# Optimization experiments

Hardware: AMD Instinct MI355X
Metric: run time of the kernel (lower is better)

## Reference

```python
import jax, jax.numpy as jnp
import numpy as np


def _cdist(a, b):
    # a: [B, N, D], b: [B, M, D] -> [B, N, M] Euclidean distances
    sq = (jnp.sum(a * a, -1)[:, :, None]
          + jnp.sum(b * b, -1)[:, None, :]
          - 2.0 * jnp.einsum('bnd,bmd->bnm', a, b))
    return jnp.sqrt(jnp.maximum(sq, 1e-12))


def setup_inputs() -> dict:
    key = jax.random.key(0)
    k1, k2, k3, k4 = jax.random.split(key, 4)
    B, N, NC, S = 2, 32768, 1024, 32
    centers = jax.random.normal(k1, (B, NC, 3), dtype=jnp.float32)
    radius = jax.random.uniform(k2, (B, NC, 1), dtype=jnp.float32)
    xyz = jax.random.normal(k3, (B, N, 3), dtype=jnp.float32)
    sphere_points = jax.random.normal(k4, (B, NC * S, 3), dtype=jnp.float32)
    return {"centers": centers, "radius": radius, "xyz": xyz,
            "sphere_points": sphere_points}


def reference(centers, radius, xyz, sphere_points):
    B, NC, _ = centers.shape
    # point -> center distances  [B, N, NC]
    dmat = _cdist(xyz, centers)
    cd_p_to_c = jnp.min(dmat, axis=-1)            # [B, N]
    idx_p_to_c = jnp.argmin(dmat, axis=-1)        # [B, N]
    # gather radius of nearest center for each point
    radius_from_p = jnp.take_along_axis(radius[..., 0], idx_p_to_c, axis=1)  # [B, N]
    # is_surface=False branch: clamp positive diffs to 0, then mean(|.|)
    diff = jnp.minimum(radius_from_p - cd_p_to_c, 0.0)
    radius_difference_p_to_c = jnp.mean(jnp.abs(diff), axis=1)               # [B]
    # sphere-point -> sample distances  [B, N, NC*S]
    dmat_sp = _cdist(xyz, sphere_points)
    cd_sp_to_p = jnp.min(dmat_sp, axis=1)          # [B, NC*S]
    max_cd_sp_to_p = jnp.max(cd_sp_to_p.reshape(B, NC, -1), axis=-1)         # [B, NC]
    radius_difference_c_to_p = jnp.mean(jnp.abs(max_cd_sp_to_p), axis=1)     # [B]
    res = radius_difference_c_to_p + radius_difference_p_to_c
    return jnp.mean(res)  # reduction='mean'
```

## Files before the change

### kernel.cpp

```cpp
#include <hip/hip_runtime.h>

#define B   2
#define N   32768
#define NC  1024
#define S   32
#define NSP (NC * S)

#define CHUNK 1024
#define NCH   (N / CHUNK)
#define BLKT  512
#define FR    4
#define COLS_BLK (8 * FR * 32)
#define GRIDX (NSP / COLS_BLK)

#define PJ  2
#define CSL 128

typedef __attribute__((ext_vector_type(8)))  short short8v;
typedef __attribute__((ext_vector_type(16))) float f32x16;
typedef const __attribute__((address_space(1))) void gvoid_t;
typedef __attribute__((address_space(3))) void svoid_t;

static __device__ __forceinline__ unsigned short f2b(float x) {
    unsigned u = __float_as_uint(x);
    return (unsigned short)((u + 0x7FFFu + ((u >> 16) & 1u)) >> 16);
}
static __device__ __forceinline__ float b2f(unsigned short u) {
    return __uint_as_float(((unsigned)u) << 16);
}
static __device__ __forceinline__ float min3f(float a, float b, float c) {
    return fminf(fminf(a, b), c);
}


__global__ __launch_bounds__(256) void k_prep(const float* __restrict__ xyz,
                                              unsigned short* __restrict__ Afrag,
                                              unsigned long long* __restrict__ best,
                                              unsigned* __restrict__ minsq,
                                              unsigned* __restrict__ accw) {
    int i = blockIdx.x * 256 + threadIdx.x;
    if (i < 2) accw[i] = 0u;
    best[i]  = ~0ull;
    minsq[i] = 0x7F800000u;

    const float* q = xyz + (size_t)i * 3;
    float qx = q[0], qy = q[1], qz = q[2];
    float h = 0.5f * (qx * qx + qy * qy + qz * qz);
    unsigned short xh = f2b(-qx), yh = f2b(-qy), zh = f2b(-qz);
    unsigned short xl = f2b(-qx - b2f(xh));
    unsigned short yl = f2b(-qy - b2f(yh));
    unsigned short zl = f2b(-qz - b2f(zh));
    unsigned short hh = f2b(h), hl = f2b(h - b2f(hh));

    int b = i >> 15, j = i & (N - 1);
    int tile = j >> 5, r = j & 31;
    unsigned short* base = Afrag + ((size_t)b * N + (size_t)tile * 32) * 16;
    uint4 s0, s1;
    s0.x = (unsigned)xh | ((unsigned)yh << 16);
    s0.y = (unsigned)zh | ((unsigned)xl << 16);
    s0.z = (unsigned)yl | ((unsigned)zl << 16);
    s0.w = (unsigned)xh | ((unsigned)yh << 16);
    s1.x = (unsigned)zh | ((unsigned)hh << 16);
    s1.y = (unsigned)hl;
    s1.z = 0u; s1.w = 0u;
    *(uint4*)(base + (size_t)r * 8)        = s0;
    *(uint4*)(base + (size_t)(r + 32) * 8) = s1;
}

__global__ __launch_bounds__(256) void k_p2c(const float* __restrict__ centers,
                                             const float* __restrict__ xyz,
                                             unsigned long long* __restrict__ best) {
    __shared__ float4 c4[CSL];
    const int b = blockIdx.z, qb = blockIdx.y, tid = threadIdx.x;

    const float* cb = centers + ((size_t)b * NC + qb * CSL) * 3;
    for (int g = tid; g < CSL / 4; g += 256) {
        float4 f0 = ((const float4*)cb)[g * 3 + 0];
        float4 f1 = ((const float4*)cb)[g * 3 + 1];
        float4 f2 = ((const float4*)cb)[g * 3 + 2];
        float x0 = f0.x, y0 = f0.y, z0 = f0.z;
        float x1 = f0.w, y1 = f1.x, z1 = f1.y;
        float x2 = f1.z, y2 = f1.w, z2 = f2.x;
        float x3 = f2.y, y3 = f2.z, z3 = f2.w;
        c4[g * 4 + 0] = make_float4(x0, y0, z0, 0.5f * (x0 * x0 + y0 * y0 + z0 * z0));
        c4[g * 4 + 1] = make_float4(x1, y1, z1, 0.5f * (x1 * x1 + y1 * y1 + z1 * z1));
        c4[g * 4 + 2] = make_float4(x2, y2, z2, 0.5f * (x2 * x2 + y2 * y2 + z2 * z2));
        c4[g * 4 + 3] = make_float4(x3, y3, z3, 0.5f * (x3 * x3 + y3 * y3 + z3 * z3));
    }
    __syncthreads();

    const int pbase = blockIdx.x * (256 * PJ) + tid;
    float px[PJ], py[PJ], pz[PJ], tmin[PJ];
    int imin[PJ];
    #pragma unroll
    for (int k = 0; k < PJ; ++k) {
        const float* p = xyz + ((size_t)b * N + pbase + k * 256) * 3;
        px[k] = p[0]; py[k] = p[1]; pz[k] = p[2];
        tmin[k] = 1e30f; imin[k] = 0;
    }

    #pragma unroll 4
    for (int c = 0; c < CSL; ++c) {
        float4 q = c4[c];
        #pragma unroll
        for (int k = 0; k < PJ; ++k) {
            float t = q.w - px[k] * q.x - py[k] * q.y - pz[k] * q.z;
            bool lt = t < tmin[k];
            tmin[k] = lt ? t : tmin[k];
            imin[k] = lt ? c : imin[k];
        }
    }

    #pragma unroll
    for (int k = 0; k < PJ; ++k) {
        unsigned bits = __float_as_uint(tmin[k]);
        unsigned ord  = (bits & 0x80000000u) ? ~bits : (bits | 0x80000000u);
        unsigned long long key =
            ((unsigned long long)ord << 32) | (unsigned)(qb * CSL + imin[k]);
        atomicMin(best + (size_t)b * N + pbase + k * 256, key);
    }
}

__global__ __launch_bounds__(BLKT) void k_sp2p(const float* __restrict__ sp,
                                               const unsigned short* __restrict__ Afrag,
                                               unsigned* __restrict__ minsq) {
    __shared__ unsigned short lds[CHUNK * 16];
    const int b = blockIdx.z, chunk = blockIdx.y;
    const int tid = threadIdx.x, wid = tid >> 6, lane = tid & 63;

    const char* src = (const char*)(Afrag +
                        ((size_t)b * N + (size_t)chunk * CHUNK) * 16);
    #pragma unroll
    for (int it = 0; it < 4; ++it) {
        int off = it * 8192 + wid * 1024;
        __builtin_amdgcn_global_load_lds((gvoid_t*)(src + off + lane * 16),
                                         (svoid_t*)((char*)lds + off), 16, 0, 0);
    }

    const int colbase = blockIdx.x * COLS_BLK + wid * (FR * 32) + (lane & 31);
    float pp[FR]; short8v bf[FR];
    #pragma unroll
    for (int f = 0; f < FR; ++f) {
        const float* p = sp + ((size_t)b * NSP + colbase + f * 32) * 3;
        float qx = p[0], qy = p[1], qz = p[2];
        pp[f] = qx * qx + qy * qy + qz * qz;
        unsigned short xh = f2b(qx), yh = f2b(qy), zh = f2b(qz);
        unsigned short xl = f2b(qx - b2f(xh));
        unsigned short yl = f2b(qy - b2f(yh));
        unsigned short zl = f2b(qz - b2f(zh));
        short8v v;
        if (lane < 32) {
            v[0] = (short)xh; v[1] = (short)yh; v[2] = (short)zh;
            v[3] = (short)xh; v[4] = (short)yh; v[5] = (short)zh;
            v[6] = (short)xl; v[7] = (short)yl;
        } else {
            v[0] = (short)zl; v[1] = (short)0x3F80; v[2] = (short)0x3F80;
            v[3] = 0; v[4] = 0; v[5] = 0; v[6] = 0; v[7] = 0;
        }
        bf[f] = v;
    }
    f32x16 zero;
    #pragma unroll
    for (int i = 0; i < 16; ++i) zero[i] = 0.0f;

    float run[FR];
    #pragma unroll
    for (int f = 0; f < FR; ++f) run[f] = 1e30f;

    __syncthreads();

    const unsigned short* ap = lds + lane * 8;
    #pragma unroll 2
    for (int t = 0; t < CHUNK / 32; ++t) {
        short8v a = *(const short8v*)(ap + (size_t)t * 512);
        #pragma unroll
        for (int f = 0; f < FR; ++f) {
            f32x16 d = __builtin_amdgcn_mfma_f32_32x32x16_bf16(a, bf[f], zero, 0, 0, 0);
            float r0 = min3f(d[0],  d[1],  d[2]);
            float r1 = min3f(d[3],  d[4],  d[5]);
            float r2 = min3f(d[6],  d[7],  d[8]);
            float r3 = min3f(d[9],  d[10], d[11]);
            float r4 = min3f(d[12], d[13], d[14]);
            float r5 = min3f(r0, r1, d[15]);
            float r6 = min3f(r2, r3, r4);
            run[f] = min3f(run[f], r5, r6);
        }
    }

    #pragma unroll
    for (int f = 0; f < FR; ++f)
        run[f] = fminf(run[f], __shfl_xor(run[f], 32, 64));
    if (lane < 32) {
        unsigned* mb = minsq + (size_t)b * NSP + colbase;
        #pragma unroll
        for (int f = 0; f < FR; ++f) {
            float sq = fmaxf(2.0f * run[f] + pp[f], 0.0f);
            atomicMin(mb + f * 32, __float_as_uint(sq));
        }
    }
}

__global__ __launch_bounds__(256) void k_fin(const unsigned long long* __restrict__ best,
                                             const unsigned* __restrict__ minsq,
                                             const float* __restrict__ xyz,
                                             const float* __restrict__ radius,
                                             float* __restrict__ acc,
                                             unsigned* __restrict__ counter,
                                             float* __restrict__ out) {
    const int tid = threadIdx.x;
    const int i = blockIdx.x * 256 + tid;
    const int b = i >> 15;

    unsigned long long k = best[i];
    int idx = (int)(k & 0xFFFFFFFFu);
    unsigned ord  = (unsigned)(k >> 32);
    unsigned bits = (ord & 0x80000000u) ? (ord ^ 0x80000000u) : ~ord;
    float tmin = __uint_as_float(bits);
    const float* p = xyz + (size_t)i * 3;
    float pp = p[0] * p[0] + p[1] * p[1] + p[2] * p[2];
    float cdp = sqrtf(fmaxf(2.0f * tmin + pp, 1e-12f));
    float val = fmaxf(cdp - radius[(size_t)b * NC + idx], 0.0f);

    float cd = sqrtf(fmaxf(__uint_as_float(minsq[i]), 1e-12f));
    #pragma unroll
    for (int o = 16; o > 0; o >>= 1) cd = fmaxf(cd, __shfl_xor(cd, o, 64));

    float contrib = val * (1.0f / N) +
                    (((tid & 31) == 0) ? cd * (1.0f / NC) : 0.0f);
    #pragma unroll
    for (int o = 32; o > 0; o >>= 1) contrib += __shfl_down(contrib, o);
    __shared__ float wsum[4];
    if ((tid & 63) == 0) wsum[tid >> 6] = contrib;
    __syncthreads();
    if (tid == 0) atomicAdd(&acc[0], wsum[0] + wsum[1] + wsum[2] + wsum[3]);

    __shared__ int lastf;
    if (tid == 0) {
        __threadfence();
        unsigned old = atomicAdd(counter, 1u);
        lastf = (old == (unsigned)(gridDim.x - 1));
    }
    __syncthreads();
    if (lastf && tid == 0)
        out[0] = atomicAdd(&acc[0], 0.0f) * (1.0f / B);
}

extern "C" void kernel_launch(void* const* d_in, const int* in_sizes, int n_in,
                              void* d_out, int out_size, void* d_ws, size_t ws_size,
                              hipStream_t stream) {
    const float* centers = (const float*)d_in[0];
    const float* radius  = (const float*)d_in[1];
    const float* xyz     = (const float*)d_in[2];
    const float* sp      = (const float*)d_in[3];
    float* out = (float*)d_out;

    unsigned short*     Afrag = (unsigned short*)d_ws;
    unsigned long long* best  = (unsigned long long*)((char*)d_ws + (size_t)B * N * 32);
    unsigned* minsq  = (unsigned*)((char*)best + (size_t)B * N * 8);
    float*    acc    = (float*)((char*)minsq + (size_t)B * NSP * 4);
    unsigned* counter = (unsigned*)acc + 1;

    hipLaunchKernelGGL(k_prep, dim3(B * N / 256), dim3(256), 0, stream,
                       xyz, Afrag, best, minsq, (unsigned*)acc);
    hipLaunchKernelGGL(k_p2c, dim3(N / (256 * PJ), NC / CSL, B), dim3(256), 0, stream,
                       centers, xyz, best);
    hipLaunchKernelGGL(k_sp2p, dim3(GRIDX, NCH, B), dim3(BLKT), 0, stream,
                       sp, Afrag, minsq);
    hipLaunchKernelGGL(k_fin, dim3(B * N / 256), dim3(256), 0, stream,
                       best, minsq, xyz, radius, acc, counter, out);
}
```

Baseline: 137.5 us.

## Fuse point-to-center and sphere-point passes into one heterogeneous kernel launch

```diff
diff --git a/kernel.cpp b/kernel.cpp
--- a/kernel.cpp
+++ b/kernel.cpp
@@ -6,15 +6,14 @@
 #define S   32
 #define NSP (NC * S)
 
-#define CHUNK 1024
+#define CHUNK 512
 #define NCH   (N / CHUNK)
-#define BLKT  512
+#define BLKT  256
 #define FR    4
-#define COLS_BLK (8 * FR * 32)
+#define COLS_BLK (4 * FR * 32)
 #define GRIDX (NSP / COLS_BLK)
-
-#define PJ  2
-#define CSL 128
+#define P2C_BLOCKS (B * N / 256)
+#define SP2P_BLOCKS (GRIDX * NCH * B)
 
 typedef __attribute__((ext_vector_type(8)))  short short8v;
 typedef __attribute__((ext_vector_type(16))) float f32x16;
@@ -35,12 +34,10 @@
 
 __global__ __launch_bounds__(256) void k_prep(const float* __restrict__ xyz,
                                               unsigned short* __restrict__ Afrag,
-                                              unsigned long long* __restrict__ best,
                                               unsigned* __restrict__ minsq,
                                               unsigned* __restrict__ accw) {
     int i = blockIdx.x * 256 + threadIdx.x;
     if (i < 2) accw[i] = 0u;
-    best[i]  = ~0ull;
     minsq[i] = 0x7F800000u;
 
     const float* q = xyz + (size_t)i * 3;
@@ -67,77 +64,81 @@
     *(uint4*)(base + (size_t)(r + 32) * 8) = s1;
 }
 
-__global__ __launch_bounds__(256) void k_p2c(const float* __restrict__ centers,
-                                             const float* __restrict__ xyz,
-                                             unsigned long long* __restrict__ best) {
-    __shared__ float4 c4[CSL];
-    const int b = blockIdx.z, qb = blockIdx.y, tid = threadIdx.x;
-
-    const float* cb = centers + ((size_t)b * NC + qb * CSL) * 3;
-    for (int g = tid; g < CSL / 4; g += 256) {
-        float4 f0 = ((const float4*)cb)[g * 3 + 0];
-        float4 f1 = ((const float4*)cb)[g * 3 + 1];
-        float4 f2 = ((const float4*)cb)[g * 3 + 2];
-        float x0 = f0.x, y0 = f0.y, z0 = f0.z;
-        float x1 = f0.w, y1 = f1.x, z1 = f1.y;
-        float x2 = f1.z, y2 = f1.w, z2 = f2.x;
-        float x3 = f2.y, y3 = f2.z, z3 = f2.w;
-        c4[g * 4 + 0] = make_float4(x0, y0, z0, 0.5f * (x0 * x0 + y0 * y0 + z0 * z0));
-        c4[g * 4 + 1] = make_float4(x1, y1, z1, 0.5f * (x1 * x1 + y1 * y1 + z1 * z1));
-        c4[g * 4 + 2] = make_float4(x2, y2, z2, 0.5f * (x2 * x2 + y2 * y2 + z2 * z2));
-        c4[g * 4 + 3] = make_float4(x3, y3, z3, 0.5f * (x3 * x3 + y3 * y3 + z3 * z3));
-    }
-    __syncthreads();
-
-    const int pbase = blockIdx.x * (256 * PJ) + tid;
-    float px[PJ], py[PJ], pz[PJ], tmin[PJ];
-    int imin[PJ];
-    #pragma unroll
-    for (int k = 0; k < PJ; ++k) {
-        const float* p = xyz + ((size_t)b * N + pbase + k * 256) * 3;
-        px[k] = p[0]; py[k] = p[1]; pz[k] = p[2];
-        tmin[k] = 1e30f; imin[k] = 0;
-    }
-
-    #pragma unroll 4
-    for (int c = 0; c < CSL; ++c) {
-        float4 q = c4[c];
+__global__ __launch_bounds__(BLKT) void k_main(const float* __restrict__ centers,
+                                               const float* __restrict__ radius,
+                                               const float* __restrict__ xyz,
+                                               const float* __restrict__ sp,
+                                               const unsigned short* __restrict__ Afrag,
+                                               unsigned* __restrict__ minsq,
+                                               float* __restrict__ acc) {
+    __shared__ union {
+        unsigned short afr[CHUNK * 16];
+        struct { float4 c4[NC]; float rad[NC]; } pc;
+    } sm;
+    const int tid = threadIdx.x, wid = tid >> 6, lane = tid & 63;
+
+    if (blockIdx.x < P2C_BLOCKS) {
+        const int g = blockIdx.x * 256 + tid;
+        const int b = g >> 15;
+        const float* cb = centers + (size_t)b * NC * 3;
+        for (int t4 = tid; t4 < NC / 4; t4 += 256) {
+            float4 f0 = ((const float4*)cb)[t4 * 3 + 0];
+            float4 f1 = ((const float4*)cb)[t4 * 3 + 1];
+            float4 f2 = ((const float4*)cb)[t4 * 3 + 2];
+            float x0 = f0.x, y0 = f0.y, z0 = f0.z;
+            float x1 = f0.w, y1 = f1.x, z1 = f1.y;
+            float x2 = f1.z, y2 = f1.w, z2 = f2.x;
+            float x3 = f2.y, y3 = f2.z, z3 = f2.w;
+            sm.pc.c4[t4 * 4 + 0] = make_float4(x0, y0, z0, 0.5f * (x0 * x0 + y0 * y0 + z0 * z0));
+            sm.pc.c4[t4 * 4 + 1] = make_float4(x1, y1, z1, 0.5f * (x1 * x1 + y1 * y1 + z1 * z1));
+            sm.pc.c4[t4 * 4 + 2] = make_float4(x2, y2, z2, 0.5f * (x2 * x2 + y2 * y2 + z2 * z2));
+            sm.pc.c4[t4 * 4 + 3] = make_float4(x3, y3, z3, 0.5f * (x3 * x3 + y3 * y3 + z3 * z3));
+        }
+        {
+            const float* rb = radius + (size_t)b * NC;
+            float4 r4 = ((const float4*)rb)[tid];
+            sm.pc.rad[tid * 4 + 0] = r4.x; sm.pc.rad[tid * 4 + 1] = r4.y;
+            sm.pc.rad[tid * 4 + 2] = r4.z; sm.pc.rad[tid * 4 + 3] = r4.w;
+        }
+        __syncthreads();
+
+        const float* p = xyz + (size_t)g * 3;
+        const float px = p[0], py = p[1], pz = p[2];
+        const float pp = px * px + py * py + pz * pz;
+        float tmin = 1e30f;
+        int   imin = 0;
+        #pragma unroll 4
+        for (int c = 0; c < NC; ++c) {
+            float4 q = sm.pc.c4[c];
+            float  t = q.w - px * q.x - py * q.y - pz * q.z;
+            if (t < tmin) { tmin = t; imin = c; }
+        }
+        const float cd = sqrtf(fmaxf(2.0f * tmin + pp, 1e-12f));
+        float contrib = fmaxf(cd - sm.pc.rad[imin], 0.0f) * (1.0f / N);
         #pragma unroll
-        for (int k = 0; k < PJ; ++k) {
-            float t = q.w - px[k] * q.x - py[k] * q.y - pz[k] * q.z;
-            bool lt = t < tmin[k];
-            tmin[k] = lt ? t : tmin[k];
-            imin[k] = lt ? c : imin[k];
-        }
-    }
-
-    #pragma unroll
-    for (int k = 0; k < PJ; ++k) {
-        unsigned bits = __float_as_uint(tmin[k]);
-        unsigned ord  = (bits & 0x80000000u) ? ~bits : (bits | 0x80000000u);
-        unsigned long long key =
-            ((unsigned long long)ord << 32) | (unsigned)(qb * CSL + imin[k]);
-        atomicMin(best + (size_t)b * N + pbase + k * 256, key);
-    }
-}
-
-__global__ __launch_bounds__(BLKT) void k_sp2p(const float* __restrict__ sp,
-                                               const unsigned short* __restrict__ Afrag,
-                                               unsigned* __restrict__ minsq) {
-    __shared__ unsigned short lds[CHUNK * 16];
-    const int b = blockIdx.z, chunk = blockIdx.y;
-    const int tid = threadIdx.x, wid = tid >> 6, lane = tid & 63;
+        for (int o = 32; o > 0; o >>= 1) contrib += __shfl_down(contrib, o);
+        __shared__ float wsum[4];
+        if (lane == 0) wsum[wid] = contrib;
+        __syncthreads();
+        if (tid == 0) atomicAdd(acc, wsum[0] + wsum[1] + wsum[2] + wsum[3]);
+        return;
+    }
+
+    const int sbid  = blockIdx.x - P2C_BLOCKS;
+    const int ct    = sbid & (GRIDX - 1);
+    const int chunk = (sbid >> 6) & (NCH - 1);
+    const int b     = sbid >> 12;
 
     const char* src = (const char*)(Afrag +
                         ((size_t)b * N + (size_t)chunk * CHUNK) * 16);
     #pragma unroll
     for (int it = 0; it < 4; ++it) {
-        int off = it * 8192 + wid * 1024;
+        int off = it * 4096 + wid * 1024;
         __builtin_amdgcn_global_load_lds((gvoid_t*)(src + off + lane * 16),
-                                         (svoid_t*)((char*)lds + off), 16, 0, 0);
-    }
-
-    const int colbase = blockIdx.x * COLS_BLK + wid * (FR * 32) + (lane & 31);
+                                         (svoid_t*)((char*)sm.afr + off), 16, 0, 0);
+    }
+
+    const int colbase = ct * COLS_BLK + wid * (FR * 32) + (lane & 31);
     float pp[FR]; short8v bf[FR];
     #pragma unroll
     for (int f = 0; f < FR; ++f) {
@@ -169,7 +170,7 @@
 
     __syncthreads();
 
-    const unsigned short* ap = lds + lane * 8;
+    const unsigned short* ap = sm.afr + lane * 8;
     #pragma unroll 2
     for (int t = 0; t < CHUNK / 32; ++t) {
         short8v a = *(const short8v*)(ap + (size_t)t * 512);
@@ -200,39 +201,23 @@
     }
 }
 
-__global__ __launch_bounds__(256) void k_fin(const unsigned long long* __restrict__ best,
-                                             const unsigned* __restrict__ minsq,
-                                             const float* __restrict__ xyz,
-                                             const float* __restrict__ radius,
+__global__ __launch_bounds__(256) void k_fin(const unsigned* __restrict__ minsq,
                                              float* __restrict__ acc,
                                              unsigned* __restrict__ counter,
                                              float* __restrict__ out) {
     const int tid = threadIdx.x;
     const int i = blockIdx.x * 256 + tid;
-    const int b = i >> 15;
-
-    unsigned long long k = best[i];
-    int idx = (int)(k & 0xFFFFFFFFu);
-    unsigned ord  = (unsigned)(k >> 32);
-    unsigned bits = (ord & 0x80000000u) ? (ord ^ 0x80000000u) : ~ord;
-    float tmin = __uint_as_float(bits);
-    const float* p = xyz + (size_t)i * 3;
-    float pp = p[0] * p[0] + p[1] * p[1] + p[2] * p[2];
-    float cdp = sqrtf(fmaxf(2.0f * tmin + pp, 1e-12f));
-    float val = fmaxf(cdp - radius[(size_t)b * NC + idx], 0.0f);
-
     float cd = sqrtf(fmaxf(__uint_as_float(minsq[i]), 1e-12f));
     #pragma unroll
     for (int o = 16; o > 0; o >>= 1) cd = fmaxf(cd, __shfl_xor(cd, o, 64));
 
-    float contrib = val * (1.0f / N) +
-                    (((tid & 31) == 0) ? cd * (1.0f / NC) : 0.0f);
+    float contrib = ((tid & 31) == 0) ? cd * (1.0f / NC) : 0.0f;
     #pragma unroll
     for (int o = 32; o > 0; o >>= 1) contrib += __shfl_down(contrib, o);
     __shared__ float wsum[4];
     if ((tid & 63) == 0) wsum[tid >> 6] = contrib;
     __syncthreads();
-    if (tid == 0) atomicAdd(&acc[0], wsum[0] + wsum[1] + wsum[2] + wsum[3]);
+    if (tid == 0) atomicAdd(acc, wsum[0] + wsum[1] + wsum[2] + wsum[3]);
 
     __shared__ int lastf;
     if (tid == 0) {
@@ -242,7 +227,7 @@
     }
     __syncthreads();
     if (lastf && tid == 0)
-        out[0] = atomicAdd(&acc[0], 0.0f) * (1.0f / B);
+        out[0] = atomicAdd(acc, 0.0f) * (1.0f / B);
 }
 
 extern "C" void kernel_launch(void* const* d_in, const int* in_sizes, int n_in,
@@ -254,18 +239,15 @@
     const float* sp      = (const float*)d_in[3];
     float* out = (float*)d_out;
 
-    unsigned short*     Afrag = (unsigned short*)d_ws;
-    unsigned long long* best  = (unsigned long long*)((char*)d_ws + (size_t)B * N * 32);
-    unsigned* minsq  = (unsigned*)((char*)best + (size_t)B * N * 8);
+    unsigned short* Afrag = (unsigned short*)d_ws;
+    unsigned* minsq  = (unsigned*)((char*)d_ws + (size_t)B * N * 32);
     float*    acc    = (float*)((char*)minsq + (size_t)B * NSP * 4);
     unsigned* counter = (unsigned*)acc + 1;
 
     hipLaunchKernelGGL(k_prep, dim3(B * N / 256), dim3(256), 0, stream,
-                       xyz, Afrag, best, minsq, (unsigned*)acc);
-    hipLaunchKernelGGL(k_p2c, dim3(N / (256 * PJ), NC / CSL, B), dim3(256), 0, stream,
-                       centers, xyz, best);
-    hipLaunchKernelGGL(k_sp2p, dim3(GRIDX, NCH, B), dim3(BLKT), 0, stream,
-                       sp, Afrag, minsq);
-    hipLaunchKernelGGL(k_fin, dim3(B * N / 256), dim3(256), 0, stream,
-                       best, minsq, xyz, radius, acc, counter, out);
-}
+                       xyz, Afrag, minsq, (unsigned*)acc);
+    hipLaunchKernelGGL(k_main, dim3(P2C_BLOCKS + SP2P_BLOCKS), dim3(BLKT), 0, stream,
+                       centers, radius, xyz, sp, Afrag, minsq, acc);
+    hipLaunchKernelGGL(k_fin, dim3(B * NSP / 256), dim3(256), 0, stream,
+                       minsq, acc, counter, out);
+}
```

After: 162.9 us. +18.4%, slower.
